# Kernel optimization log

Hardware: AMD Instinct MI355X
Metric: run time of the kernel (lower is better)

The kernel has to match this reference:

```python
import jax, jax.numpy as jnp
import numpy as np

N_NODES = 50000
N_EDGES = 262144
EMBED = 512
FF = 1024
N_GRAPHS = 64
EPS = 1e-12  # F.normalize default eps


def setup_inputs() -> dict:
    key = jax.random.key(0)
    ks = jax.random.split(key, 12)
    d_in = 3 * EMBED
    s1 = 1.0 / np.sqrt(d_in)
    s2 = 1.0 / np.sqrt(FF)
    return {
        "x": jax.random.normal(ks[0], (N_NODES + N_EDGES, EMBED), jnp.float32),
        "pos": jax.random.normal(ks[1], (N_NODES, 3), jnp.float32),
        "W1e": jax.random.uniform(ks[2], (d_in, FF), jnp.float32, -s1, s1),
        "b1e": jax.random.uniform(ks[3], (FF,), jnp.float32, -s1, s1),
        "W2e": jax.random.uniform(ks[4], (FF, 1), jnp.float32, -s2, s2),
        "b2e": jax.random.uniform(ks[5], (1,), jnp.float32, -s2, s2),
        "W1f": jax.random.uniform(ks[6], (d_in, FF), jnp.float32, -s1, s1),
        "b1f": jax.random.uniform(ks[7], (FF,), jnp.float32, -s1, s1),
        "W2f": jax.random.uniform(ks[8], (FF, 1), jnp.float32, -s2, s2),
        "b2f": jax.random.uniform(ks[9], (1,), jnp.float32, -s2, s2),
        "batch": jnp.sort(jax.random.randint(ks[10], (N_NODES,), 0, N_GRAPHS, jnp.int32)),
        "edge_index": jax.random.randint(ks[11], (2, N_EDGES), 0, N_NODES, jnp.int32),
    }


def _mlp(h, W1, b1, W2, b2):
    return jax.nn.gelu(h @ W1 + b1) @ W2 + b2


def reference(x, pos, W1e, b1e, W2e, b2e, W1f, b1f, W2f, b2f, batch, edge_index):
    n_nodes = pos.shape[0]
    n_edges = edge_index.shape[1]
    src, dst = edge_index[0], edge_index[1]
    # edge-token rows of x live right after the node rows
    edge_tok = jax.lax.dynamic_slice_in_dim(x, n_nodes, n_edges, axis=0)
    inputs = jnp.concatenate([x[src], x[dst], edge_tok], axis=-1)  # [E, 3*D]
    vec = pos[src] - pos[dst]  # [E, 3]
    norm = jnp.linalg.norm(vec, axis=-1, keepdims=True)
    vec_hat = vec / jnp.maximum(norm, EPS)
    energy_pairs = _mlp(inputs, W1e, b1e, W2e, b2e)            # [E, 1]
    force_pairs = _mlp(inputs, W1f, b1f, W2f, b2f) * vec_hat   # [E, 3]
    energy = jax.ops.segment_sum(energy_pairs, batch[src], num_segments=N_GRAPHS)
    forces = jax.ops.segment_sum(force_pairs, src, num_segments=n_nodes)
    return energy, forces
```

## Files before the change

### kernel.cpp

```cpp
#include <hip/hip_runtime.h>
#include <cstdint>
#include <cstddef>

#define E_CNT   262144
#define NNODES  50000
#define EMB     512
#define KD      1536
#define ND      2048
#define NG      64
#define XROWS   (NNODES + E_CNT)

typedef unsigned short u16;
typedef short  s8v __attribute__((ext_vector_type(8)));
typedef float  f4v __attribute__((ext_vector_type(4)));

#define WS_XB   0u
#define WS_WT   319635456u
#define WS_B1   325926912u
#define WS_W2   325935104u
#define WS_P    325943296u
#define WS_END  342720512u

__device__ __forceinline__ u16 f2bf(float f) {
    union { float f; uint32_t u; } v; v.f = f;
    uint32_t u = v.u;
    return (u16)((u + 0x7FFFu + ((u >> 16) & 1u)) >> 16);
}

__global__ void cvt_x(const float* __restrict__ x, uint32_t* __restrict__ xb) {
    size_t i = ((size_t)blockIdx.x * 256 + threadIdx.x) * 8;
    float4 a = *(const float4*)(x + i);
    float4 b = *(const float4*)(x + i + 4);
    uint4 r;
    r.x = (uint32_t)f2bf(a.x) | ((uint32_t)f2bf(a.y) << 16);
    r.y = (uint32_t)f2bf(a.z) | ((uint32_t)f2bf(a.w) << 16);
    r.z = (uint32_t)f2bf(b.x) | ((uint32_t)f2bf(b.y) << 16);
    r.w = (uint32_t)f2bf(b.z) | ((uint32_t)f2bf(b.w) << 16);
    *(uint4*)((char*)xb + i * 2) = r;
}

__global__ void prep_w(const float* __restrict__ W1e, const float* __restrict__ W1f,
                       u16* __restrict__ wt) {
    __shared__ float tile[32][33];
    int n0 = blockIdx.x * 32, k0 = blockIdx.y * 32;
    int tx = threadIdx.x & 31, ty = threadIdx.x >> 5;
#pragma unroll
    for (int i = 0; i < 4; ++i) {
        int k = k0 + ty + i * 8, n = n0 + tx;
        float v = (n < 1024) ? W1e[k * 1024 + n] : W1f[k * 1024 + (n - 1024)];
        tile[ty + i * 8][tx] = v;
    }
    __syncthreads();
#pragma unroll
    for (int i = 0; i < 4; ++i) {
        int nl = ty + i * 8, kl = tx;
        wt[(size_t)(n0 + nl) * KD + k0 + kl] = f2bf(tile[kl][nl]);
    }
}

__global__ void prep_small(const float* __restrict__ b1e, const float* __restrict__ b1f,
                           const float* __restrict__ W2e, const float* __restrict__ W2f,
                           float* __restrict__ b1c, float* __restrict__ w2c) {
    int n = blockIdx.x * 256 + threadIdx.x;
    if (n < 1024) { b1c[n] = b1e[n]; w2c[n] = W2e[n]; }
    else          { b1c[n] = b1f[n - 1024]; w2c[n] = W2f[n - 1024]; }
}

__global__ __launch_bounds__(512, 2)
void gemm_mlp(const u16* __restrict__ xb, const u16* __restrict__ wt,
              const float* __restrict__ b1c, const float* __restrict__ w2c,
              const int* __restrict__ ei, float* __restrict__ P) {
    __shared__ u16 Al[3][128 * 64];
    __shared__ u16 Bl[3][256 * 64];
    __shared__ float part[128];

    const unsigned o = blockIdx.x + (blockIdx.y << 3);
    const int mb = (int)((o & 7u) + ((o >> 6) << 3));
    const int nb = (int)((o >> 3) & 7u);
    const int m0 = mb << 7;
    const int n0 = nb << 8;
    const int t  = threadIdx.x;
    const int l  = t & 63;
    const int w  = t >> 6;

    const int lr    = l >> 3;
    const int unit  = l & 7;
    const int sunit = (unit ^ lr) << 3;

    int srcs[2], dsts[2];
#pragma unroll
    for (int i = 0; i < 2; ++i) {
        int e = m0 + i * 64 + w * 8 + lr;
        srcs[i] = ei[e];
        dsts[i] = ei[E_CNT + e];
    }

    if (t < 128) part[t] = 0.0f;

    const int wm = (w & 1) << 6;
    const int wn = (w >> 1) << 6;
    const int l15 = l & 15;

    float b1v[4], w2v[4];
#pragma unroll
    for (int nf = 0; nf < 4; ++nf) {
        int n = n0 + wn + nf * 16 + l15;
        b1v[nf] = b1c[n];
        w2v[nf] = w2c[n];
    }

    f4v acc[4][4];
#pragma unroll
    for (int mf = 0; mf < 4; ++mf)
#pragma unroll
        for (int nf = 0; nf < 4; ++nf)
            acc[mf][nf] = (f4v){0.f, 0.f, 0.f, 0.f};

    auto stage = [&](u16* Ad, u16* Bd, int kt) {
        const int k0   = kt << 6;
        const int seg  = k0 >> 9;
        const int koff = k0 & 511;
#pragma unroll
        for (int i = 0; i < 2; ++i) {
            int row;
            if (seg == 0)      row = srcs[i];
            else if (seg == 1) row = dsts[i];
            else               row = NNODES + m0 + i * 64 + w * 8 + lr;
            const u16* g = xb + (size_t)row * EMB + koff + sunit;
            __builtin_amdgcn_global_load_lds(
                (const __attribute__((address_space(1))) void*)g,
                (__attribute__((address_space(3))) void*)(Ad + (i * 64 + w * 8) * 64),
                16, 0, 0);
        }
#pragma unroll
        for (int j = 0; j < 4; ++j) {
            int n = n0 + j * 64 + w * 8 + lr;
            const u16* g = wt + (size_t)n * KD + k0 + sunit;
            __builtin_amdgcn_global_load_lds(
                (const __attribute__((address_space(1))) void*)g,
                (__attribute__((address_space(3))) void*)(Bd + (j * 64 + w * 8) * 64),
                16, 0, 0);
        }
    };

    const int po0 = (((l >> 4) ^ (l & 7)) << 3);
    const int po1 = (((4 | (l >> 4)) ^ (l & 7)) << 3);

    auto compute = [&](const u16* Ab, const u16* Bb) {
        s8v a[2][4], b[2][4];
#pragma unroll
        for (int mf = 0; mf < 4; ++mf) {
            a[0][mf] = *(const s8v*)(Ab + (wm + mf * 16 + l15) * 64 + po0);
            a[1][mf] = *(const s8v*)(Ab + (wm + mf * 16 + l15) * 64 + po1);
        }
#pragma unroll
        for (int nf = 0; nf < 4; ++nf) {
            b[0][nf] = *(const s8v*)(Bb + (wn + nf * 16 + l15) * 64 + po0);
            b[1][nf] = *(const s8v*)(Bb + (wn + nf * 16 + l15) * 64 + po1);
        }
        __builtin_amdgcn_s_setprio(1);
#pragma unroll
        for (int ks = 0; ks < 2; ++ks)
#pragma unroll
            for (int mf = 0; mf < 4; ++mf)
#pragma unroll
                for (int nf = 0; nf < 4; ++nf)
                    acc[mf][nf] = __builtin_amdgcn_mfma_f32_16x16x32_bf16(
                        a[ks][mf], b[ks][nf], acc[mf][nf], 0, 0, 0);
        __builtin_amdgcn_s_setprio(0);
    };

    u16 *Ac = Al[0], *An = Al[1], *As = Al[2];
    u16 *Bc = Bl[0], *Bn = Bl[1], *Bs = Bl[2];

    stage(Ac, Bc, 0);
    stage(An, Bn, 1);
    __syncthreads();

    stage(As, Bs, 2);
    compute(Ac, Bc);
    { u16* tA = Ac; Ac = An; An = As; As = tA;
      u16* tB = Bc; Bc = Bn; Bn = Bs; Bs = tB; }

    for (int kt = 1; kt <= 21; ++kt) {
        asm volatile("s_waitcnt vmcnt(6)" ::: "memory");
        __builtin_amdgcn_s_barrier();
        stage(As, Bs, kt + 2);
        compute(Ac, Bc);
        { u16* tA = Ac; Ac = An; An = As; As = tA;
          u16* tB = Bc; Bc = Bn; Bn = Bs; Bs = tB; }
    }
    asm volatile("s_waitcnt vmcnt(6)" ::: "memory");
    __builtin_amdgcn_s_barrier();
    compute(Ac, Bc);
    { u16* tA = Ac; Ac = An; An = As; As = tA;
      u16* tB = Bc; Bc = Bn; Bn = Bs; Bs = tB; }
    asm volatile("s_waitcnt vmcnt(0)" ::: "memory");
    __builtin_amdgcn_s_barrier();
    compute(Ac, Bc);

#pragma unroll
    for (int mf = 0; mf < 4; ++mf) {
#pragma unroll
        for (int r = 0; r < 4; ++r) {
            float s = 0.f;
#pragma unroll
            for (int nf = 0; nf < 4; ++nf) {
                float h  = acc[mf][nf][r] + b1v[nf];
                float x2 = h * h;
                float pp = fmaf(x2, 0.044715f, 1.0f);
                float u2 = 1.5957691216f * h * pp;
                float ex = __expf(-u2);
                float sg = __builtin_amdgcn_rcpf(1.0f + ex);
                s = fmaf(h * sg, w2v[nf], s);
            }
            s += __shfl_xor(s, 1);
            s += __shfl_xor(s, 2);
            s += __shfl_xor(s, 4);
            s += __shfl_xor(s, 8);
            if ((l & 15) == 0) {
                int m = wm + mf * 16 + ((l >> 4) << 2) + r;
                atomicAdd(&part[m], s);
            }
        }
    }
    __syncthreads();
    if (t < 128) P[(size_t)nb * E_CNT + m0 + t] = part[t];
}

__global__ void finalize(const float* __restrict__ P, const int* __restrict__ ei,
                         const float* __restrict__ pos, const int* __restrict__ batch,
                         const float* __restrict__ b2e, const float* __restrict__ b2f,
                         float* __restrict__ out) {
    __shared__ float ebin[NG];
    int t = threadIdx.x;
    if (t < NG) ebin[t] = 0.f;
    __syncthreads();
    int e = blockIdx.x * 256 + t;

    float se = b2e[0], sf = b2f[0];
#pragma unroll
    for (int nb = 0; nb < 4; ++nb)  se += P[(size_t)nb * E_CNT + e];
#pragma unroll
    for (int nb = 4; nb < 8; ++nb)  sf += P[(size_t)nb * E_CNT + e];

    int s = ei[e], d = ei[E_CNT + e];
    float vx = pos[3 * s]     - pos[3 * d];
    float vy = pos[3 * s + 1] - pos[3 * d + 1];
    float vz = pos[3 * s + 2] - pos[3 * d + 2];
    float nrm = sqrtf(vx * vx + vy * vy + vz * vz);
    float inv = sf / fmaxf(nrm, 1e-12f);
    atomicAdd(&out[NG + 3 * s],     vx * inv);
    atomicAdd(&out[NG + 3 * s + 1], vy * inv);
    atomicAdd(&out[NG + 3 * s + 2], vz * inv);
    atomicAdd(&ebin[batch[s]], se);

    __syncthreads();
    if (t < NG) {
        float v = ebin[t];
        if (v != 0.f) atomicAdd(&out[t], v);
    }
}

extern "C" void kernel_launch(void* const* d_in, const int* in_sizes, int n_in,
                              void* d_out, int out_size, void* d_ws, size_t ws_size,
                              hipStream_t stream) {
    const float* x    = (const float*)d_in[0];
    const float* pos  = (const float*)d_in[1];
    const float* W1e  = (const float*)d_in[2];
    const float* b1e  = (const float*)d_in[3];
    const float* W2e  = (const float*)d_in[4];
    const float* b2e  = (const float*)d_in[5];
    const float* W1f  = (const float*)d_in[6];
    const float* b1f  = (const float*)d_in[7];
    const float* W2f  = (const float*)d_in[8];
    const float* b2f  = (const float*)d_in[9];
    const int*  batch = (const int*)d_in[10];
    const int*  ei    = (const int*)d_in[11];
    float* out        = (float*)d_out;

    if (ws_size < (size_t)WS_END) return;

    char* ws = (char*)d_ws;
    uint32_t* xb32 = (uint32_t*)(ws + WS_XB);
    u16*      xb   = (u16*)(ws + WS_XB);
    u16*      wt   = (u16*)(ws + WS_WT);
    float*    b1c  = (float*)(ws + WS_B1);
    float*    w2c  = (float*)(ws + WS_W2);
    float*    P    = (float*)(ws + WS_P);

    hipMemsetAsync(d_out, 0, (size_t)out_size * sizeof(float), stream);

    cvt_x<<<78036, 256, 0, stream>>>(x, xb32);
    prep_w<<<dim3(64, 48), 256, 0, stream>>>(W1e, W1f, wt);
    prep_small<<<8, 256, 0, stream>>>(b1e, b1f, W2e, W2f, b1c, w2c);
    gemm_mlp<<<dim3(8, 2048), 512, 0, stream>>>(xb, wt, b1c, w2c, ei, P);
    finalize<<<1024, 256, 0, stream>>>(P, ei, pos, batch, b2e, b2f, out);
}
```

Baseline: 2.634 ms.

## Widen GEMM tile to 128x512 with K=32 stages and remap block order

The fused gather-GEMM-GELU kernel now computes a 128x512 output tile per block instead of 128x256. K steps shrink from 64 to 32 so LDS stays the same size, and each wave holds 4x8 MFMA accumulators. Gathered x rows are loaded once per four N-tiles rather than per eight, which halves redundant A traffic and the partial-sum buffer P that finalize reads. The costs are twice the accumulator registers, which may hurt occupancy at launch_bounds(512,2), and twice as many pipeline iterations with less compute per barrier. Block ordering is also remapped so that the N-tiles for the same edges are scheduled close together.

```diff
diff --git a/kernel.cpp b/kernel.cpp
--- a/kernel.cpp
+++ b/kernel.cpp
@@ -70,103 +70,90 @@
 void gemm_mlp(const u16* __restrict__ xb, const u16* __restrict__ wt,
               const float* __restrict__ b1c, const float* __restrict__ w2c,
               const int* __restrict__ ei, float* __restrict__ P) {
-    __shared__ u16 Al[3][128 * 64];
-    __shared__ u16 Bl[3][256 * 64];
+    __shared__ u16 Al[3][128 * 32];
+    __shared__ u16 Bl[3][512 * 32];
     __shared__ float part[128];
 
-    const unsigned o = blockIdx.x + (blockIdx.y << 3);
-    const int mb = (int)((o & 7u) + ((o >> 6) << 3));
-    const int nb = (int)((o >> 3) & 7u);
+    const unsigned o = blockIdx.x + (blockIdx.y << 2);
+    const unsigned g = (o & 7u) * 1024u + (o >> 3);
+    const int mb = (int)(g >> 2);
+    const int nb = (int)(g & 3u);
     const int m0 = mb << 7;
-    const int n0 = nb << 8;
+    const int n0 = nb << 9;
     const int t  = threadIdx.x;
     const int l  = t & 63;
     const int w  = t >> 6;
 
-    const int lr    = l >> 3;
-    const int unit  = l & 7;
-    const int sunit = (unit ^ lr) << 3;
-
-    int srcs[2], dsts[2];
-#pragma unroll
-    for (int i = 0; i < 2; ++i) {
-        int e = m0 + i * 64 + w * 8 + lr;
-        srcs[i] = ei[e];
-        dsts[i] = ei[E_CNT + e];
-    }
+    const int sunit = (((l & 3) ^ ((l >> 3) & 3)) << 3);
+    const int rA    = (t >> 2);
+
+    const int srcA = ei[m0 + rA];
+    const int dstA = ei[E_CNT + m0 + rA];
 
     if (t < 128) part[t] = 0.0f;
 
     const int wm = (w & 1) << 6;
-    const int wn = (w >> 1) << 6;
+    const int wn = (w >> 1) << 7;
     const int l15 = l & 15;
 
-    float b1v[4], w2v[4];
-#pragma unroll
-    for (int nf = 0; nf < 4; ++nf) {
+    float b1v[8], w2v[8];
+#pragma unroll
+    for (int nf = 0; nf < 8; ++nf) {
         int n = n0 + wn + nf * 16 + l15;
         b1v[nf] = b1c[n];
         w2v[nf] = w2c[n];
     }
 
-    f4v acc[4][4];
+    f4v acc[4][8];
 #pragma unroll
     for (int mf = 0; mf < 4; ++mf)
 #pragma unroll
-        for (int nf = 0; nf < 4; ++nf)
+        for (int nf = 0; nf < 8; ++nf)
             acc[mf][nf] = (f4v){0.f, 0.f, 0.f, 0.f};
 
     auto stage = [&](u16* Ad, u16* Bd, int kt) {
-        const int k0   = kt << 6;
+        const int k0   = kt << 5;
         const int seg  = k0 >> 9;
         const int koff = k0 & 511;
-#pragma unroll
-        for (int i = 0; i < 2; ++i) {
+        {
             int row;
-            if (seg == 0)      row = srcs[i];
-            else if (seg == 1) row = dsts[i];
-            else               row = NNODES + m0 + i * 64 + w * 8 + lr;
-            const u16* g = xb + (size_t)row * EMB + koff + sunit;
+            if (seg == 0)      row = srcA;
+            else if (seg == 1) row = dstA;
+            else               row = NNODES + m0 + rA;
+            const u16* gp = xb + (size_t)row * EMB + koff + sunit;
             __builtin_amdgcn_global_load_lds(
-                (const __attribute__((address_space(1))) void*)g,
-                (__attribute__((address_space(3))) void*)(Ad + (i * 64 + w * 8) * 64),
+                (const __attribute__((address_space(1))) void*)gp,
+                (__attribute__((address_space(3))) void*)(Ad + w * 512),
                 16, 0, 0);
         }
 #pragma unroll
         for (int j = 0; j < 4; ++j) {
-            int n = n0 + j * 64 + w * 8 + lr;
-            const u16* g = wt + (size_t)n * KD + k0 + sunit;
+            int n = n0 + j * 128 + (rA & 15) + (w << 4);
+            const u16* gp = wt + (size_t)n * KD + k0 + sunit;
             __builtin_amdgcn_global_load_lds(
-                (const __attribute__((address_space(1))) void*)g,
-                (__attribute__((address_space(3))) void*)(Bd + (j * 64 + w * 8) * 64),
+                (const __attribute__((address_space(1))) void*)gp,
+                (__attribute__((address_space(3))) void*)(Bd + j * 4096 + w * 512),
                 16, 0, 0);
         }
     };
 
-    const int po0 = (((l >> 4) ^ (l & 7)) << 3);
-    const int po1 = (((4 | (l >> 4)) ^ (l & 7)) << 3);
+    const int po = (((l >> 4) ^ ((l15 >> 1) & 3)) << 3);
 
     auto compute = [&](const u16* Ab, const u16* Bb) {
-        s8v a[2][4], b[2][4];
-#pragma unroll
-        for (int mf = 0; mf < 4; ++mf) {
-            a[0][mf] = *(const s8v*)(Ab + (wm + mf * 16 + l15) * 64 + po0);
-            a[1][mf] = *(const s8v*)(Ab + (wm + mf * 16 + l15) * 64 + po1);
-        }
-#pragma unroll
-        for (int nf = 0; nf < 4; ++nf) {
-            b[0][nf] = *(const s8v*)(Bb + (wn + nf * 16 + l15) * 64 + po0);
-            b[1][nf] = *(const s8v*)(Bb + (wn + nf * 16 + l15) * 64 + po1);
-        }
+        s8v a[4], b[8];
+#pragma unroll
+        for (int mf = 0; mf < 4; ++mf)
+            a[mf] = *(const s8v*)(Ab + (wm + mf * 16 + l15) * 32 + po);
+#pragma unroll
+        for (int nf = 0; nf < 8; ++nf)
+            b[nf] = *(const s8v*)(Bb + (wn + nf * 16 + l15) * 32 + po);
         __builtin_amdgcn_s_setprio(1);
 #pragma unroll
-        for (int ks = 0; ks < 2; ++ks)
-#pragma unroll
-            for (int mf = 0; mf < 4; ++mf)
-#pragma unroll
-                for (int nf = 0; nf < 4; ++nf)
-                    acc[mf][nf] = __builtin_amdgcn_mfma_f32_16x16x32_bf16(
-                        a[ks][mf], b[ks][nf], acc[mf][nf], 0, 0, 0);
+        for (int mf = 0; mf < 4; ++mf)
+#pragma unroll
+            for (int nf = 0; nf < 8; ++nf)
+                acc[mf][nf] = __builtin_amdgcn_mfma_f32_16x16x32_bf16(
+                    a[mf], b[nf], acc[mf][nf], 0, 0, 0);
         __builtin_amdgcn_s_setprio(0);
     };
 
@@ -182,15 +169,15 @@
     { u16* tA = Ac; Ac = An; An = As; As = tA;
       u16* tB = Bc; Bc = Bn; Bn = Bs; Bs = tB; }
 
-    for (int kt = 1; kt <= 21; ++kt) {
-        asm volatile("s_waitcnt vmcnt(6)" ::: "memory");
+    for (int kt = 1; kt <= 45; ++kt) {
+        asm volatile("s_waitcnt vmcnt(5)" ::: "memory");
         __builtin_amdgcn_s_barrier();
         stage(As, Bs, kt + 2);
         compute(Ac, Bc);
         { u16* tA = Ac; Ac = An; An = As; As = tA;
           u16* tB = Bc; Bc = Bn; Bn = Bs; Bs = tB; }
     }
-    asm volatile("s_waitcnt vmcnt(6)" ::: "memory");
+    asm volatile("s_waitcnt vmcnt(5)" ::: "memory");
     __builtin_amdgcn_s_barrier();
     compute(Ac, Bc);
     { u16* tA = Ac; Ac = An; An = As; As = tA;
@@ -205,7 +192,7 @@
         for (int r = 0; r < 4; ++r) {
             float s = 0.f;
 #pragma unroll
-            for (int nf = 0; nf < 4; ++nf) {
+            for (int nf = 0; nf < 8; ++nf) {
                 float h  = acc[mf][nf][r] + b1v[nf];
                 float x2 = h * h;
                 float pp = fmaf(x2, 0.044715f, 1.0f);
@@ -238,11 +225,8 @@
     __syncthreads();
     int e = blockIdx.x * 256 + t;
 
-    float se = b2e[0], sf = b2f[0];
-#pragma unroll
-    for (int nb = 0; nb < 4; ++nb)  se += P[(size_t)nb * E_CNT + e];
-#pragma unroll
-    for (int nb = 4; nb < 8; ++nb)  sf += P[(size_t)nb * E_CNT + e];
+    float se = b2e[0] + P[e] + P[(size_t)1 * E_CNT + e];
+    float sf = b2f[0] + P[(size_t)2 * E_CNT + e] + P[(size_t)3 * E_CNT + e];
 
     int s = ei[e], d = ei[E_CNT + e];
     float vx = pos[3 * s]     - pos[3 * d];
@@ -294,6 +278,6 @@
     cvt_x<<<78036, 256, 0, stream>>>(x, xb32);
     prep_w<<<dim3(64, 48), 256, 0, stream>>>(W1e, W1f, wt);
     prep_small<<<8, 256, 0, stream>>>(b1e, b1f, W2e, W2f, b1c, w2c);
-    gemm_mlp<<<dim3(8, 2048), 512, 0, stream>>>(xb, wt, b1c, w2c, ei, P);
+    gemm_mlp<<<dim3(4, 2048), 512, 0, stream>>>(xb, wt, b1c, w2c, ei, P);
     finalize<<<1024, 256, 0, stream>>>(P, ei, pos, batch, b2e, b2f, out);
 }
```

Result: no change. 2.677 ms (+1.7%).
